# Performance work log

Hardware: AMD Instinct MI355X
Metric: run time of the kernel (lower is better)

## Reference

```python
import jax, jax.numpy as jnp
import numpy as np
import math

DIM = 512
BLOCK_NUM = 16
SEQ_LEN = 8192
BLOCK_LEN = SEQ_LEN // BLOCK_NUM  # 512 == DIM -> mask used as-is
BATCH = 4
LN_EPS = 1e-3  # keras LayerNormalization default epsilon


def setup_inputs() -> dict:
    key = jax.random.key(0)
    ks = jax.random.split(key, 5)
    inputs = jax.random.normal(ks[0], (BATCH, BLOCK_NUM, BLOCK_LEN, DIM), dtype=jnp.float32)
    # binary padding-style mask, values in {0,1}
    mask_array = jax.random.randint(ks[1], (BATCH, SEQ_LEN, DIM), 0, 2).astype(jnp.float32)
    scale = 1.0 / math.sqrt(DIM)
    dw1 = jax.random.normal(ks[2], (DIM, DIM), dtype=jnp.float32) * scale
    dw2 = jax.random.normal(ks[3], (DIM, DIM), dtype=jnp.float32) * scale
    dw3 = jax.random.normal(ks[4], (DIM, DIM), dtype=jnp.float32) * scale
    db1 = jnp.zeros((DIM,), dtype=jnp.float32)
    db2 = jnp.zeros((DIM,), dtype=jnp.float32)
    db3 = jnp.zeros((DIM,), dtype=jnp.float32)
    return {"inputs": inputs, "mask_array": mask_array,
            "dw1": dw1, "dw2": dw2, "dw3": dw3,
            "db1": db1, "db2": db2, "db3": db3}


def reference(inputs, mask_array, dw1, dw2, dw3, db1, db2, db3):
    # inputs: [B, block_num, block_len, dim]
    Q = jnp.matmul(inputs, dw1) + db1
    K = jnp.matmul(inputs, dw2) + db2
    V = jnpp_matmul = jnp.matmul(inputs, dw3) + db3
    V = jnp.matmul(inputs, dw3) + db3
    # block-local attention scores: [B, bn, bl, bl]
    scores = jnp.einsum('bnqd,bnkd->bnqk', Q, K) / math.sqrt(DIM)
    # mask: [B, seq_len, dim] -> [B, bn, bl, dim]; block_len == dim so no slice/tile
    m = mask_array.reshape(BATCH, BLOCK_NUM, BLOCK_LEN, DIM)
    scores = scores + (1.0 - m) * jnp.float32(-1e10)
    p = jax.nn.softmax(scores, axis=-1)
    out = jnp.einsum('bnqk,bnkd->bnqd', p, V) + inputs  # residual
    # LayerNorm(axis=-1), fresh keras layer: gamma=1, beta=0, eps=1e-3
    mean = jnp.mean(out, axis=-1, keepdims=True)
    var = jnp.mean(jnp.square(out - mean), axis=-1, keepdims=True)
    return (out - mean) / jnp.sqrt(var + LN_EPS)
```

## Files before the change

### kernel.cpp

```cpp
#include <hip/hip_runtime.h>

#define DIMK 512
#define NBLK 64
#define NTOK 32768

typedef short  short8 __attribute__((ext_vector_type(8)));
typedef float  f32x4  __attribute__((ext_vector_type(4)));
typedef unsigned short u16x8 __attribute__((ext_vector_type(8)));

__device__ __forceinline__ unsigned short f2bf(float f) {
  union { float f; unsigned u; } v; v.f = f;
  unsigned r = (v.u + 0x7FFFu + ((v.u >> 16) & 1u)) >> 16;
  return (unsigned short)r;
}
__device__ __forceinline__ float bf2f(unsigned short h) {
  return __uint_as_float(((unsigned)h) << 16);
}

__device__ __forceinline__ void gload_lds16(const unsigned short* g,
                                            unsigned short* l) {
  __builtin_amdgcn_global_load_lds(
      (const __attribute__((address_space(1))) unsigned int*)(g),
      (__attribute__((address_space(3))) unsigned int*)(l),
      16, 0, 0);
}

__device__ __forceinline__ int swz(int c) { return c ^ ((c >> 3) & 3); }


__global__ __launch_bounds__(256) void k_prep(
    const float* __restrict__ X, const float* __restrict__ mask,
    const float* __restrict__ dw1, const float* __restrict__ dw2,
    const float* __restrict__ dw3,
    unsigned short* __restrict__ Xb, unsigned char* __restrict__ bits,
    unsigned short* __restrict__ Wt)
{
  __shared__ float t[64][65];
  const int b = blockIdx.x;
  const int tid = threadIdx.x;
  if (b < 8192) {
    const size_t gid = (size_t)b * 256 + tid;
    const size_t i = gid * 8;
    const int tok = (int)(i >> 9);
    const int col = (int)(i & 511);
    const float4 a = *(const float4*)(X + i);
    const float4 bb = *(const float4*)(X + i + 4);
    u16x8 o;
    o[0] = f2bf(a.x); o[1] = f2bf(a.y); o[2] = f2bf(a.z); o[3] = f2bf(a.w);
    o[4] = f2bf(bb.x); o[5] = f2bf(bb.y); o[6] = f2bf(bb.z); o[7] = f2bf(bb.w);
    *(u16x8*)(Xb + ((size_t)(tok >> 7) * 16 + (col >> 5)) * 4096 +
              (tok & 127) * 32 + (col & 31)) = o;
  } else if (b < 16384) {
    const size_t gid = (size_t)(b - 8192) * 256 + tid;
    const size_t i = gid * 8;
    const float4 ma = *(const float4*)(mask + i);
    const float4 mb = *(const float4*)(mask + i + 4);
    unsigned v = 0;
    v |= (ma.x > 0.5f) << 0; v |= (ma.y > 0.5f) << 1;
    v |= (ma.z > 0.5f) << 2; v |= (ma.w > 0.5f) << 3;
    v |= (mb.x > 0.5f) << 4; v |= (mb.y > 0.5f) << 5;
    v |= (mb.z > 0.5f) << 6; v |= (mb.w > 0.5f) << 7;
    bits[gid] = (unsigned char)v;
  } else {
    const int bb = b - 16384;
    const int w = bb >> 6;
    const int tt = bb & 63;
    const int kt = (tt >> 3) * 64;
    const int nt = (tt & 7) * 64;
    const float* dw = (w == 0) ? dw1 : (w == 1) ? dw2 : dw3;
    const int rr = tid >> 4;
    const int cc = (tid & 15) << 2;
#pragma unroll
    for (int p = 0; p < 4; ++p) {
      const int r = rr + p * 16;
      const float4 v = *(const float4*)&dw[(size_t)(kt + r) * 512 + nt + cc];
      t[cc + 0][r] = v.x; t[cc + 1][r] = v.y;
      t[cc + 2][r] = v.z; t[cc + 3][r] = v.w;
    }
    __syncthreads();
#pragma unroll
    for (int p = 0; p < 4; ++p) {
      const int r = rr + p * 16;
      const int n = nt + r;
      const int k = kt + cc;
      ushort4 o;
      o.x = f2bf(t[r][cc + 0]); o.y = f2bf(t[r][cc + 1]);
      o.z = f2bf(t[r][cc + 2]); o.w = f2bf(t[r][cc + 3]);
      *(ushort4*)&Wt[(size_t)w * 262144 + (size_t)(k >> 5) * 16384 +
                     (size_t)n * 32 + (k & 31)] = o;
    }
  }
}

__global__ __launch_bounds__(256, 2) void k_qkv(
    const unsigned short* __restrict__ Xb, const unsigned short* __restrict__ Wt,
    const float* __restrict__ db1, const float* __restrict__ db2,
    const float* __restrict__ db3,
    unsigned short* __restrict__ Qb, unsigned short* __restrict__ Kb,
    unsigned short* __restrict__ Vt)
{
  __shared__ __align__(16) unsigned short smem[32768];

  const int id = blockIdx.x;
  const int x = id & 7, j = id >> 3;
  const int mtile = x * 32 + (j >> 2);
  const int nt = j & 3;
  const int m0 = mtile * 128;
  const int n0 = nt * 128;

  const int tid = threadIdx.x, lane = tid & 63, wv = tid >> 6;
  const int quad = lane >> 4, l16 = lane & 15;
  const int qx = quad ^ ((l16 >> 1) & 3);
  const int rb = (wv >> 1) * 64, cb = (wv & 1) * 64;

  f32x4 acc[3][4][4];
#pragma unroll
  for (int w = 0; w < 3; ++w)
#pragma unroll
    for (int i = 0; i < 4; ++i)
#pragma unroll
      for (int jj = 0; jj < 4; ++jj) {
        f32x4 z = {0.f, 0.f, 0.f, 0.f}; acc[w][i][jj] = z;
      }

  auto stage = [&](unsigned short* base, int it) {
    const unsigned short* aslab = Xb + ((size_t)mtile * 16 + it) * 4096;
    gload_lds16(aslab + swz(tid) * 8, base + tid * 8);
    gload_lds16(aslab + swz(tid + 256) * 8, base + (tid + 256) * 8);
#pragma unroll
    for (int h = 0; h < 6; ++h) {
      const int c = tid + h * 256;
      const int w = c >> 9, cc = c & 511;
      const unsigned short* bslab =
          Wt + (size_t)w * 262144 + (size_t)it * 16384 + (size_t)n0 * 32;
      gload_lds16(bslab + swz(cc) * 8, base + 4096 + w * 4096 + cc * 8);
    }
  };

  stage(smem, 0);
  __syncthreads();
  int cur = 0;
  for (int it = 0; it < 16; ++it) {
    unsigned short* cbuf = smem + cur * 16384;
    if (it < 15) stage(smem + (cur ^ 1) * 16384, it + 1);
    const unsigned short* As = cbuf;
    const unsigned short* Bs = cbuf + 4096;
    short8 af[4];
#pragma unroll
    for (int i = 0; i < 4; ++i)
      af[i] = *(const short8*)&As[(rb + i * 16 + l16) * 32 + qx * 8];
#pragma unroll
    for (int jj = 0; jj < 4; ++jj)
#pragma unroll
      for (int w = 0; w < 3; ++w) {
        const short8 bf =
            *(const short8*)&Bs[w * 4096 + (cb + jj * 16 + l16) * 32 + qx * 8];
#pragma unroll
        for (int i = 0; i < 4; ++i)
          acc[w][i][jj] = __builtin_amdgcn_mfma_f32_16x16x32_bf16(
              af[i], bf, acc[w][i][jj], 0, 0, 0);
      }
    __syncthreads();
    cur ^= 1;
  }

#pragma unroll
  for (int w = 0; w < 2; ++w) {
    __syncthreads();
    const float* db = (w == 0) ? db1 : db2;
#pragma unroll
    for (int i = 0; i < 4; ++i)
#pragma unroll
      for (int jj = 0; jj < 4; ++jj) {
        const int cl = cb + jj * 16 + l16;
        const float bv = db[n0 + cl];
        const int t0 = rb + i * 16 + quad * 4;
#pragma unroll
        for (int r = 0; r < 4; ++r)
          smem[(t0 + r) * 144 + cl] = f2bf(acc[w][i][jj][r] + bv);
      }
    __syncthreads();
#pragma unroll
    for (int h = 0; h < 8; ++h) {
      const int c = tid + h * 256;
      const int tl = c >> 4, c0 = (c & 15) * 8;
      const int tokg = m0 + tl, colg = n0 + c0;
      const u16x8 v = *(const u16x8*)&smem[tl * 144 + c0];
      if (w == 0)
        *(u16x8*)&Qb[((size_t)(tokg >> 6) * 16 + (colg >> 5)) * 2048 +
                     (tokg & 63) * 32 + (colg & 31)] = v;
      else
        *(u16x8*)&Kb[((size_t)(tokg >> 9) * 16 + (colg >> 5)) * 16384 +
                     (tokg & 511) * 32 + (colg & 31)] = v;
    }
  }
  __syncthreads();
#pragma unroll
  for (int i = 0; i < 4; ++i)
#pragma unroll
    for (int jj = 0; jj < 4; ++jj) {
      const int cl = cb + jj * 16 + l16;
      const int t0 = rb + i * 16 + quad * 4;
      const float bv = db3[n0 + cl];
      ushort4 pk;
      pk.x = f2bf(acc[2][i][jj][0] + bv);
      pk.y = f2bf(acc[2][i][jj][1] + bv);
      pk.z = f2bf(acc[2][i][jj][2] + bv);
      pk.w = f2bf(acc[2][i][jj][3] + bv);
      *(ushort4*)&smem[cl * 136 + t0] = pk;
    }
  __syncthreads();
#pragma unroll
  for (int h = 0; h < 8; ++h) {
    const int c = tid + h * 256;
    const int cl = c >> 4, toff = (c & 15) * 8;
    const int tg = mtile * 128 + toff;
    *(u16x8*)&Vt[(size_t)(tg >> 5) * 16384 + (size_t)(n0 + cl) * 32 +
                 (tg & 31)] = *(const u16x8*)&smem[cl * 136 + toff];
  }
}

__global__ __launch_bounds__(256, 2) void k_attn_p(
    const unsigned short* __restrict__ Qb, const unsigned short* __restrict__ Kb,
    const unsigned long long* __restrict__ bits, unsigned short* __restrict__ Pb)
{
  __shared__ __align__(16) unsigned short smem[36864];
  __shared__ float red[4][64];
  const int tid = threadIdx.x, lane = tid & 63, wv = tid >> 6;
  const int quad = lane >> 4, l16 = lane & 15;
  const int qx = quad ^ ((l16 >> 1) & 3);
  const int blk = blockIdx.x & 63, mt = blockIdx.x >> 6;
  const size_t q0 = (size_t)blk * 512 + (size_t)mt * 64;
  const int qt = blk * 8 + mt;

  f32x4 acc[4][8];
#pragma unroll
  for (int i = 0; i < 4; ++i)
#pragma unroll
    for (int j = 0; j < 8; ++j) { f32x4 z = {0.f, 0.f, 0.f, 0.f}; acc[i][j] = z; }

  auto stage = [&](unsigned short* base, int it) {
    const unsigned short* aslab = Qb + ((size_t)qt * 16 + it) * 2048;
    gload_lds16(aslab + swz(tid) * 8, base + tid * 8);
    const unsigned short* bslab = Kb + ((size_t)blk * 16 + it) * 16384;
#pragma unroll
    for (int h = 0; h < 8; ++h) {
      const int c = tid + h * 256;
      gload_lds16(bslab + swz(c) * 8, base + 2048 + c * 8);
    }
  };

  stage(smem, 0);
  __syncthreads();
  int cur = 0;
  for (int it = 0; it < 16; ++it) {
    unsigned short* cbuf = smem + cur * 18432;
    if (it < 15) stage(smem + (cur ^ 1) * 18432, it + 1);
    const unsigned short* As = cbuf;
    const unsigned short* Bs = cbuf + 2048;
    short8 af[4], bfv[8];
#pragma unroll
    for (int i = 0; i < 4; ++i)
      af[i] = *(const short8*)&As[(i * 16 + l16) * 32 + qx * 8];
#pragma unroll
    for (int j = 0; j < 8; ++j)
      bfv[j] = *(const short8*)&Bs[(wv * 128 + j * 16 + l16) * 32 + qx * 8];
#pragma unroll
    for (int i = 0; i < 4; ++i)
#pragma unroll
      for (int j = 0; j < 8; ++j)
        acc[i][j] = __builtin_amdgcn_mfma_f32_16x16x32_bf16(
            af[i], bfv[j], acc[i][j], 0, 0, 0);
    __syncthreads();
    cur ^= 1;
  }

  const float scale = 0.04419417382415922f;
  float rmax[4][4];
#pragma unroll
  for (int i = 0; i < 4; ++i)
#pragma unroll
    for (int r = 0; r < 4; ++r) rmax[i][r] = -3.0e38f;
#pragma unroll
  for (int i = 0; i < 4; ++i)
#pragma unroll
    for (int r = 0; r < 4; ++r) {
      const size_t tok = q0 + i * 16 + quad * 4 + r;
      const unsigned long long w0 = bits[tok * 8 + wv * 2];
      const unsigned long long w1 = bits[tok * 8 + wv * 2 + 1];
#pragma unroll
      for (int j = 0; j < 8; ++j) {
        const unsigned long long sel = (j < 4) ? w0 : w1;
        const float bias = ((sel >> (l16 + 16 * (j & 3))) & 1ull) ? 0.0f : -1e10f;
        const float v = acc[i][j][r] * scale + bias;
        acc[i][j][r] = v;
        rmax[i][r] = fmaxf(rmax[i][r], v);
      }
    }
#pragma unroll
  for (int i = 0; i < 4; ++i)
#pragma unroll
    for (int r = 0; r < 4; ++r)
      for (int d = 1; d < 16; d <<= 1)
        rmax[i][r] = fmaxf(rmax[i][r], __shfl_xor(rmax[i][r], d, 64));
  if (l16 == 0)
#pragma unroll
    for (int i = 0; i < 4; ++i)
#pragma unroll
      for (int r = 0; r < 4; ++r) red[wv][i * 16 + quad * 4 + r] = rmax[i][r];
  __syncthreads();
#pragma unroll
  for (int i = 0; i < 4; ++i)
#pragma unroll
    for (int r = 0; r < 4; ++r) {
      const int row = i * 16 + quad * 4 + r;
      rmax[i][r] = fmaxf(fmaxf(red[0][row], red[1][row]),
                         fmaxf(red[2][row], red[3][row]));
    }
  __syncthreads();
  float rsum[4][4];
#pragma unroll
  for (int i = 0; i < 4; ++i)
#pragma unroll
    for (int r = 0; r < 4; ++r) rsum[i][r] = 0.f;
#pragma unroll
  for (int i = 0; i < 4; ++i)
#pragma unroll
    for (int j = 0; j < 8; ++j)
#pragma unroll
      for (int r = 0; r < 4; ++r) {
        const float e = __expf(acc[i][j][r] - rmax[i][r]);
        acc[i][j][r] = e;
        rsum[i][r] += e;
      }
#pragma unroll
  for (int i = 0; i < 4; ++i)
#pragma unroll
    for (int r = 0; r < 4; ++r)
      for (int d = 1; d < 16; d <<= 1)
        rsum[i][r] += __shfl_xor(rsum[i][r], d, 64);
  if (l16 == 0)
#pragma unroll
    for (int i = 0; i < 4; ++i)
#pragma unroll
      for (int r = 0; r < 4; ++r) red[wv][i * 16 + quad * 4 + r] = rsum[i][r];
  __syncthreads();
#pragma unroll
  for (int i = 0; i < 4; ++i)
#pragma unroll
    for (int r = 0; r < 4; ++r) {
      const int row = i * 16 + quad * 4 + r;
      rsum[i][r] = 1.0f / (red[0][row] + red[1][row] + red[2][row] + red[3][row]);
    }
#pragma unroll
  for (int i = 0; i < 4; ++i)
#pragma unroll
    for (int j = 0; j < 8; ++j) {
      const int cl = wv * 128 + j * 16 + l16;
      const int t0 = i * 16 + quad * 4;
#pragma unroll
      for (int r = 0; r < 4; ++r)
        smem[(t0 + r) * 528 + cl] = f2bf(acc[i][j][r] * rsum[i][r]);
    }
  __syncthreads();
#pragma unroll
  for (int h = 0; h < 16; ++h) {
    const int c = tid + h * 256;
    const int tl = c >> 6, c0 = (c & 63) * 8;
    const int tokg = (int)q0 + tl;
    const u16x8 v = *(const u16x8*)&smem[tl * 528 + c0];
    *(u16x8*)&Pb[((size_t)(tokg >> 6) * 16 + (c0 >> 5)) * 2048 +
                 (tokg & 63) * 32 + (c0 & 31)] = v;
  }
}

__global__ __launch_bounds__(256, 2) void k_pv_ln(
    const unsigned short* __restrict__ Pb, const unsigned short* __restrict__ Vt,
    const unsigned short* __restrict__ Xb, float* __restrict__ Out)
{
  __shared__ __align__(16) unsigned short smem[36864];
  __shared__ float2 red[4][64];
  const int tid = threadIdx.x, lane = tid & 63, wv = tid >> 6;
  const int quad = lane >> 4, l16 = lane & 15;
  const int qx = quad ^ ((l16 >> 1) & 3);
  const int blk = blockIdx.x & 63, mt = blockIdx.x >> 6;
  const size_t q0 = (size_t)blk * 512 + (size_t)mt * 64;
  const int qt = blk * 8 + mt;

  f32x4 acc[4][8];
#pragma unroll
  for (int i = 0; i < 4; ++i)
#pragma unroll
    for (int j = 0; j < 8; ++j) { f32x4 z = {0.f, 0.f, 0.f, 0.f}; acc[i][j] = z; }

  auto stage = [&](unsigned short* base, int it) {
    const unsigned short* aslab = Pb + ((size_t)qt * 16 + it) * 2048;
    gload_lds16(aslab + swz(tid) * 8, base + tid * 8);
    const unsigned short* bslab = Vt + ((size_t)blk * 16 + it) * 16384;
#pragma unroll
    for (int h = 0; h < 8; ++h) {
      const int c = tid + h * 256;
      gload_lds16(bslab + swz(c) * 8, base + 2048 + c * 8);
    }
  };

  stage(smem, 0);
  __syncthreads();
  int cur = 0;
  for (int it = 0; it < 16; ++it) {
    unsigned short* cbuf = smem + cur * 18432;
    if (it < 15) stage(smem + (cur ^ 1) * 18432, it + 1);
    const unsigned short* As = cbuf;
    const unsigned short* Bs = cbuf + 2048;
    short8 af[4], bfv[8];
#pragma unroll
    for (int i = 0; i < 4; ++i)
      af[i] = *(const short8*)&As[(i * 16 + l16) * 32 + qx * 8];
#pragma unroll
    for (int j = 0; j < 8; ++j)
      bfv[j] = *(const short8*)&Bs[(wv * 128 + j * 16 + l16) * 32 + qx * 8];
#pragma unroll
    for (int i = 0; i < 4; ++i)
#pragma unroll
      for (int j = 0; j < 8; ++j)
        acc[i][j] = __builtin_amdgcn_mfma_f32_16x16x32_bf16(
            af[i], bfv[j], acc[i][j], 0, 0, 0);
    __syncthreads();
    cur ^= 1;
  }

  float vsum[4][4], vsq[4][4];
#pragma unroll
  for (int i = 0; i < 4; ++i)
#pragma unroll
    for (int r = 0; r < 4; ++r) { vsum[i][r] = 0.f; vsq[i][r] = 0.f; }
#pragma unroll
  for (int i = 0; i < 4; ++i)
#pragma unroll
    for (int j = 0; j < 8; ++j)
#pragma unroll
      for (int r = 0; r < 4; ++r) {
        const int tok = (int)(q0 + i * 16 + quad * 4 + r);
        const int col = wv * 128 + j * 16 + l16;
        const float v = acc[i][j][r] +
            bf2f(Xb[((size_t)(tok >> 7) * 16 + (col >> 5)) * 4096 +
                    (tok & 127) * 32 + (col & 31)]);
        acc[i][j][r] = v;
        vsum[i][r] += v;
        vsq[i][r] += v * v;
      }
#pragma unroll
  for (int i = 0; i < 4; ++i)
#pragma unroll
    for (int r = 0; r < 4; ++r)
      for (int d = 1; d < 16; d <<= 1) {
        vsum[i][r] += __shfl_xor(vsum[i][r], d, 64);
        vsq[i][r]  += __shfl_xor(vsq[i][r], d, 64);
      }
  if (l16 == 0)
#pragma unroll
    for (int i = 0; i < 4; ++i)
#pragma unroll
      for (int r = 0; r < 4; ++r) {
        float2 p; p.x = vsum[i][r]; p.y = vsq[i][r];
        red[wv][i * 16 + quad * 4 + r] = p;
      }
  __syncthreads();
#pragma unroll
  for (int i = 0; i < 4; ++i)
#pragma unroll
    for (int r = 0; r < 4; ++r) {
      const int row = i * 16 + quad * 4 + r;
      float s = 0.f, q = 0.f;
#pragma unroll
      for (int w = 0; w < 4; ++w) { s += red[w][row].x; q += red[w][row].y; }
      const float mean = s * (1.0f / 512.0f);
      const float var  = q * (1.0f / 512.0f) - mean * mean;
      vsum[i][r] = mean;
      vsq[i][r]  = rsqrtf(var + 1e-3f);
    }
  float* L = (float*)smem;
#pragma unroll
  for (int p = 0; p < 2; ++p) {
    __syncthreads();
    if ((wv >> 1) == p) {
#pragma unroll
      for (int i = 0; i < 4; ++i)
#pragma unroll
        for (int j = 0; j < 8; ++j) {
          const int cl = (wv & 1) * 128 + j * 16 + l16;
          const int t0 = i * 16 + quad * 4;
#pragma unroll
          for (int r = 0; r < 4; ++r)
            L[(t0 + r) * 264 + cl] = (acc[i][j][r] - vsum[i][r]) * vsq[i][r];
        }
    }
    __syncthreads();
#pragma unroll
    for (int h = 0; h < 16; ++h) {
      const int c = tid + h * 256;
      const int tl = c >> 6, c0 = (c & 63) * 4;
      const float4 v = *(const float4*)&L[tl * 264 + c0];
      *(float4*)&Out[(q0 + tl) * (size_t)DIMK + p * 256 + c0] = v;
    }
  }
}

extern "C" void kernel_launch(void* const* d_in, const int* in_sizes, int n_in,
                              void* d_out, int out_size, void* d_ws, size_t ws_size,
                              hipStream_t stream)
{
  const float* X    = (const float*)d_in[0];
  const float* mask = (const float*)d_in[1];
  const float* dw1  = (const float*)d_in[2];
  const float* dw2  = (const float*)d_in[3];
  const float* dw3  = (const float*)d_in[4];
  const float* db1  = (const float*)d_in[5];
  const float* db2  = (const float*)d_in[6];
  const float* db3  = (const float*)d_in[7];
  float* Out = (float*)d_out;

  char* ws = (char*)d_ws;
  const size_t MB = 1ull << 20;
  unsigned short* Wt = (unsigned short*)(ws);
  unsigned short* Qb = (unsigned short*)(ws + 2 * MB);
  unsigned short* Kb = (unsigned short*)(ws + 34 * MB);
  unsigned short* Vt = (unsigned short*)(ws + 66 * MB);
  unsigned short* Xb = (unsigned short*)(ws + 98 * MB);
  unsigned short* Pb = Qb;
  unsigned char*  bits = (unsigned char*)d_out;

  k_prep   <<<16576, 256, 0, stream>>>(X, mask, dw1, dw2, dw3, Xb, bits, Wt);
  k_qkv    <<<1024, 256, 0, stream>>>(Xb, Wt, db1, db2, db3, Qb, Kb, Vt);
  k_attn_p <<<512, 256, 0, stream>>>(Qb, Kb, (const unsigned long long*)bits, Pb);
  k_pv_ln  <<<512, 256, 0, stream>>>(Pb, Vt, Xb, Out);
}
```

Before: 294.6 us.

## Write Q/K directly from registers, remap block ids, change LDS padding strides

The QKV projection epilogue no longer stages Q and K through shared memory. Each lane now writes scalar bf16 values straight into the tiled global layouts, which removes several barriers and the LDS round trip but replaces coalesced 16-byte stores with scattered 2-byte stores. The attention and PV/LayerNorm kernels remap blockIdx so that consecutive workgroups land on different attention blocks, which may change cache and channel locality. The LDS row paddings for the P and output staging buffers are also reduced (528 to 520 and 264 to 260), which alters the bank-conflict patterns.

```diff
diff --git a/kernel.cpp b/kernel.cpp
--- a/kernel.cpp
+++ b/kernel.cpp
@@ -165,36 +165,18 @@
   }
 
 #pragma unroll
-  for (int w = 0; w < 2; ++w) {
-    __syncthreads();
-    const float* db = (w == 0) ? db1 : db2;
-#pragma unroll
-    for (int i = 0; i < 4; ++i)
-#pragma unroll
-      for (int jj = 0; jj < 4; ++jj) {
-        const int cl = cb + jj * 16 + l16;
-        const float bv = db[n0 + cl];
-        const int t0 = rb + i * 16 + quad * 4;
-#pragma unroll
-        for (int r = 0; r < 4; ++r)
-          smem[(t0 + r) * 144 + cl] = f2bf(acc[w][i][jj][r] + bv);
-      }
-    __syncthreads();
-#pragma unroll
-    for (int h = 0; h < 8; ++h) {
-      const int c = tid + h * 256;
-      const int tl = c >> 4, c0 = (c & 15) * 8;
-      const int tokg = m0 + tl, colg = n0 + c0;
-      const u16x8 v = *(const u16x8*)&smem[tl * 144 + c0];
-      if (w == 0)
-        *(u16x8*)&Qb[((size_t)(tokg >> 6) * 16 + (colg >> 5)) * 2048 +
-                     (tokg & 63) * 32 + (colg & 31)] = v;
-      else
-        *(u16x8*)&Kb[((size_t)(tokg >> 9) * 16 + (colg >> 5)) * 16384 +
-                     (tokg & 511) * 32 + (colg & 31)] = v;
-    }
-  }
-  __syncthreads();
+  for (int i = 0; i < 4; ++i)
+#pragma unroll
+    for (int jj = 0; jj < 4; ++jj)
+#pragma unroll
+      for (int r = 0; r < 4; ++r) {
+        const int tok = m0 + rb + i * 16 + quad * 4 + r;
+        const int col = n0 + cb + jj * 16 + l16;
+        Qb[((size_t)(tok >> 6) * 16 + (col >> 5)) * 2048 +
+           (tok & 63) * 32 + (col & 31)] = f2bf(acc[0][i][jj][r] + db1[col]);
+        Kb[((size_t)(tok >> 9) * 16 + (col >> 5)) * 16384 +
+           (tok & 511) * 32 + (col & 31)] = f2bf(acc[1][i][jj][r] + db2[col]);
+      }
 #pragma unroll
   for (int i = 0; i < 4; ++i)
 #pragma unroll
@@ -229,7 +211,9 @@
   const int tid = threadIdx.x, lane = tid & 63, wv = tid >> 6;
   const int quad = lane >> 4, l16 = lane & 15;
   const int qx = quad ^ ((l16 >> 1) & 3);
-  const int blk = blockIdx.x & 63, mt = blockIdx.x >> 6;
+  const int id = blockIdx.x;
+  const int blk = (id & 7) * 8 + ((id >> 3) & 7);
+  const int mt = id >> 6;
   const size_t q0 = (size_t)blk * 512 + (size_t)mt * 64;
   const int qt = blk * 8 + mt;
 
@@ -360,7 +344,7 @@
       const int t0 = i * 16 + quad * 4;
 #pragma unroll
       for (int r = 0; r < 4; ++r)
-        smem[(t0 + r) * 528 + cl] = f2bf(acc[i][j][r] * rsum[i][r]);
+        smem[(t0 + r) * 520 + cl] = f2bf(acc[i][j][r] * rsum[i][r]);
     }
   __syncthreads();
 #pragma unroll
@@ -368,7 +352,7 @@
     const int c = tid + h * 256;
     const int tl = c >> 6, c0 = (c & 63) * 8;
     const int tokg = (int)q0 + tl;
-    const u16x8 v = *(const u16x8*)&smem[tl * 528 + c0];
+    const u16x8 v = *(const u16x8*)&smem[tl * 520 + c0];
     *(u16x8*)&Pb[((size_t)(tokg >> 6) * 16 + (c0 >> 5)) * 2048 +
                  (tokg & 63) * 32 + (c0 & 31)] = v;
   }
@@ -383,7 +367,9 @@
   const int tid = threadIdx.x, lane = tid & 63, wv = tid >> 6;
   const int quad = lane >> 4, l16 = lane & 15;
   const int qx = quad ^ ((l16 >> 1) & 3);
-  const int blk = blockIdx.x & 63, mt = blockIdx.x >> 6;
+  const int id = blockIdx.x;
+  const int blk = (id & 7) * 8 + ((id >> 3) & 7);
+  const int mt = id >> 6;
   const size_t q0 = (size_t)blk * 512 + (size_t)mt * 64;
   const int qt = blk * 8 + mt;
 
@@ -492,7 +478,7 @@
           const int t0 = i * 16 + quad * 4;
 #pragma unroll
           for (int r = 0; r < 4; ++r)
-            L[(t0 + r) * 264 + cl] = (acc[i][j][r] - vsum[i][r]) * vsq[i][r];
+            L[(t0 + r) * 260 + cl] = (acc[i][j][r] - vsum[i][r]) * vsq[i][r];
         }
     }
     __syncthreads();
@@ -500,7 +486,7 @@
     for (int h = 0; h < 16; ++h) {
       const int c = tid + h * 256;
       const int tl = c >> 6, c0 = (c & 63) * 4;
-      const float4 v = *(const float4*)&L[tl * 264 + c0];
+      const float4 v = *(const float4*)&L[tl * 260 + c0];
       *(float4*)&Out[(q0 + tl) * (size_t)DIMK + p * 256 + c0] = v;
     }
   }
```

Result: no change. 291.9 us (-0.9%).
